# Kernel tuning notes

Measured on AMD Instinct MI355X. Metric: run time of the kernel, lower is better.

The kernel has to match this reference:

```python
import jax, jax.numpy as jnp
import numpy as np

B, L, S = 128, 80, 8          # dialogues, utterances per dialogue, speakers
NODE_DIM, HIDDEN, HEADS, OUT_DIM = 768, 512, 8, 256
N = B * L


def _build_edges():
    """Replicates InterSentenceGNN.build_graph + Batch.from_data_list offsets."""
    rel = np.zeros((N, 3), np.float32)
    all_e, last = [], []
    eye3 = np.eye(3, dtype=np.float32)
    for b in range(B):
        off = b * L
        u = L - 1
        e, t = [], []
        for i in range(L):
            if i > 0:
                e += [[i - 1, i], [i, i - 1]]; t += [0, 0]   # REL_SEQ
            if i < u:
                e += [[i, u], [u, i]]; t += [1, 1]           # REL_CTX
        for s in range(S):                                   # REL_SPK, round-robin speakers
            g = list(range(s, L, S))
            for a in range(len(g)):
                for c in range(a + 1, len(g)):
                    e += [[g[a], g[c]], [g[c], g[a]]]; t += [2, 2]
        e = np.asarray(e, np.int64); t = np.asarray(t, np.int64)
        np.add.at(rel, e[:, 0] + off, eye3[t])               # out-degree per relation (pre-unique)
        all_e.append(np.unique(e, axis=0) + off)             # torch.unique(idx, dim=1)
        last.append(off + u)
    edge_index = np.concatenate(all_e, 0).T.astype(np.int32)  # [2, E], row0=src, row1=dst
    return edge_index, rel, np.asarray(last, np.int32)


def setup_inputs() -> dict:
    key = jax.random.key(0)
    ks = jax.random.split(key, 16)
    edge_index, rel_feat, last_idx = _build_edges()
    g = lambda k, shp, fan: jax.random.normal(k, shp, jnp.float32) * (1.0 / np.sqrt(fan))
    return {
        "x": jax.random.normal(ks[0], (N, NODE_DIM), jnp.float32),
        "rel_feat": jnp.asarray(rel_feat),
        "w1": g(ks[1], (3, 64), 3), "b1": jnp.zeros((64,), jnp.float32),
        "w2": g(ks[2], (64, 1), 64), "b2": jnp.zeros((1,), jnp.float32),
        "Wl1": g(ks[3], (NODE_DIM, HIDDEN), NODE_DIM), "bl1": jnp.zeros((HIDDEN,), jnp.float32),
        "Wr1": g(ks[4], (NODE_DIM, HIDDEN), NODE_DIM), "br1": jnp.zeros((HIDDEN,), jnp.float32),
        "att1": g(ks[5], (HEADS, HIDDEN // HEADS), HIDDEN // HEADS),
        "bias1": jnp.zeros((HIDDEN,), jnp.float32),
        "Wl2": g(ks[6], (HIDDEN, OUT_DIM), HIDDEN), "bl2": jnp.zeros((OUT_DIM,), jnp.float32),
        "Wr2": g(ks[7], (HIDDEN, OUT_DIM), HIDDEN), "br2": jnp.zeros((OUT_DIM,), jnp.float32),
        "att2": g(ks[8], (1, OUT_DIM), OUT_DIM),
        "bias2": jnp.zeros((OUT_DIM,), jnp.float32),
        "ln_g": jnp.ones((OUT_DIM,), jnp.float32), "ln_b": jnp.zeros((OUT_DIM,), jnp.float32),
        "edge_index": jnp.asarray(edge_index),
        "last_idx": jnp.asarray(last_idx),
    }


def _gatv2(x, Wl, bl, Wr, br, att, bias, src, dst, heads, ch, concat):
    """PyG GATv2Conv (eval mode, self-loops already in src/dst)."""
    n = x.shape[0]
    xl = (x @ Wl + bl).reshape(n, heads, ch)   # source transform (messages)
    xr = (x @ Wr + br).reshape(n, heads, ch)   # target transform
    e = jax.nn.leaky_relu(xl[src] + xr[dst], negative_slope=0.2)  # [E,H,C]
    logit = jnp.einsum("ehc,hc->eh", e, att)                      # [E,H]
    m = jax.ops.segment_max(logit, dst, num_segments=n)
    a = jnp.exp(logit - m[dst])
    denom = jax.ops.segment_sum(a, dst, num_segments=n)
    alpha = a / denom[dst]                                        # segment softmax over dst
    msg = (xl[src] * alpha[:, :, None]).reshape(-1, heads * ch)
    out = jax.ops.segment_sum(msg, dst, num_segments=n).reshape(n, heads, ch)
    out = out.reshape(n, heads * ch) if concat else out.mean(axis=1)
    return out + bias


def reference(x, rel_feat, w1, b1, w2, b2, Wl1, bl1, Wr1, br1, att1, bias1,
              Wl2, bl2, Wr2, br2, att2, bias2, ln_g, ln_b, edge_index, last_idx):
    n = x.shape[0]
    loops = jnp.arange(n, dtype=edge_index.dtype)
    src = jnp.concatenate([edge_index[0], loops])  # add_self_loops=True (PyG default)
    dst = jnp.concatenate([edge_index[1], loops])
    w = jax.nn.sigmoid(jax.nn.relu(rel_feat @ w1 + b1) @ w2 + b2)  # [N,1] node gate
    h = x * w
    h = jax.nn.elu(_gatv2(h, Wl1, bl1, Wr1, br1, att1, bias1, src, dst, HEADS, HIDDEN // HEADS, True))
    h = _gatv2(h, Wl2, bl2, Wr2, br2, att2, bias2, src, dst, 1, OUT_DIM, False)
    mu = jnp.mean(h, axis=-1, keepdims=True)
    var = jnp.mean((h - mu) ** 2, axis=-1, keepdims=True)
    h = (h - mu) * jax.lax.rsqrt(var + 1e-5) * ln_g + ln_b
    return h[last_idx]  # x[batch.ptr[1:] - 1]: last (context) node per dialogue
```

## Files before the change

### kernel.cpp

```cpp
#include <hip/hip_runtime.h>
#include <hip/hip_bf16.h>

#define NN 10240
#define LL 80
#define BB 128

typedef _Float16 half8 __attribute__((ext_vector_type(8)));
typedef _Float16 half2v __attribute__((ext_vector_type(2)));
typedef float f32x4 __attribute__((ext_vector_type(4)));

#define GLD16(gptr, lptr)                                                        \
  __builtin_amdgcn_global_load_lds(                                              \
      (const __attribute__((address_space(1))) void*)(gptr),                     \
      (__attribute__((address_space(3))) void*)(lptr), 16, 0, 0)

__device__ __forceinline__ float dot2f(half2v a, half2v b, float c) {
#if __has_builtin(__builtin_amdgcn_fdot2)
  return __builtin_amdgcn_fdot2(a, b, c, false);
#else
  return c + (float)a.x * (float)b.x + (float)a.y * (float)b.y;
#endif
}
__device__ __forceinline__ half2v u2h(unsigned int u) { half2v r; __builtin_memcpy(&r, &u, 4); return r; }
__device__ __forceinline__ unsigned int h2u(half2v h) { unsigned int u; __builtin_memcpy(&u, &h, 4); return u; }
__device__ __forceinline__ unsigned int dupf16(float v) {
  _Float16 hv = (_Float16)v;
  unsigned short u; __builtin_memcpy(&u, &hv, 2);
  return (unsigned int)u * 0x10001u;
}

__global__ __launch_bounds__(256) void prep_all(
    const float* __restrict__ x, const float* __restrict__ rel,
    const float* __restrict__ w1, const float* __restrict__ b1,
    const float* __restrict__ w2, const float* __restrict__ b2,
    const float* __restrict__ Wl1, const float* __restrict__ Wr1,
    const float* __restrict__ Wl2, const float* __restrict__ Wr2,
    const float* __restrict__ bl1, const float* __restrict__ br1,
    const float* __restrict__ att1,
    _Float16* __restrict__ h0, _Float16* __restrict__ Wt1,
    _Float16* __restrict__ Wt2cat,
    float* __restrict__ biasc, _Float16* __restrict__ att_h) {
  __shared__ float tile[32][33];
  int bid = blockIdx.x;
  int tid = threadIdx.x;
  if (bid < NN) {
    int n = bid;
    __shared__ float s_w;
    if (tid < 64) {
      float r0 = rel[n * 3 + 0], r1 = rel[n * 3 + 1], r2 = rel[n * 3 + 2];
      float v = r0 * w1[tid] + r1 * w1[64 + tid] + r2 * w1[128 + tid] + b1[tid];
      v = v > 0.f ? v : 0.f;
      v *= w2[tid];
      for (int d = 32; d; d >>= 1) v += __shfl_down(v, d, 64);
      if (tid == 0) s_w = 1.f / (1.f + __expf(-(v + b2[0])));
    }
    __syncthreads();
    float w = s_w;
    const float* xr = x + (size_t)n * 768;
    _Float16* hr = h0 + (size_t)n * 768;
    for (int c = tid; c < 768; c += 256) hr[c] = (_Float16)(xr[c] * w);
    return;
  }
  int r = bid - NN;
  const float* W;
  _Float16* Wt;
  int K, Nc, bx, by;
  if (r < 384)      { W = Wl1; Wt = Wt1;                          K = 768; Nc = 512; bx = r % 16;       by = r / 16; }
  else if (r < 768) { W = Wr1; Wt = Wt1 + (size_t)512 * 768;      K = 768; Nc = 512; bx = (r-384) % 16; by = (r-384) / 16; }
  else if (r < 896) { W = Wl2; Wt = Wt2cat;                       K = 512; Nc = 256; bx = (r-768) % 8;  by = (r-768) / 8; }
  else if (r < 1024){ W = Wr2; Wt = Wt2cat + (size_t)256 * 512;   K = 512; Nc = 256; bx = (r-896) % 8;  by = (r-896) / 8; }
  else {
    for (int i = tid; i < 1024; i += 256) biasc[i] = (i < 512) ? bl1[i] : br1[i - 512];
    for (int i = tid; i < 512; i += 256) att_h[i] = (_Float16)att1[i];
    return;
  }
  int n0 = bx * 32, k0 = by * 32;
  int c = tid & 31, rr = tid >> 5;
#pragma unroll
  for (int p = 0; p < 4; ++p) {
    int rw = p * 8 + rr;
    tile[rw][c] = W[(size_t)(k0 + rw) * Nc + n0 + c];
  }
  __syncthreads();
#pragma unroll
  for (int p = 0; p < 4; ++p) {
    int rw = p * 8 + rr;
    Wt[(size_t)(n0 + rw) * K + k0 + c] = (_Float16)tile[c][rw];
  }
}

__global__ __launch_bounds__(256) void gemm_mfma(
    const _Float16* __restrict__ A, const _Float16* __restrict__ Bt,
    const float* __restrict__ bias, _Float16* __restrict__ Cout,
    int K, int Nc) {
  __shared__ __align__(16) _Float16 As[128 * 32];
  __shared__ __align__(16) _Float16 Bs[128 * 32];
  int bm = blockIdx.y * 128, bn = blockIdx.x * 128;
  int tid = threadIdx.x;
  int wave = tid >> 6, lane = tid & 63;
  int wm = (wave & 1) * 64, wn = (wave >> 1) * 64;
  int lr = lane & 15, lk = lane >> 4;
  int r0 = tid >> 2, sg = tid & 3;
  const _Float16* aP0 = A + (size_t)(bm + r0) * K + sg * 8;
  const _Float16* aP1 = A + (size_t)(bm + 64 + r0) * K + sg * 8;
  const _Float16* bP0 = Bt + (size_t)(bn + r0) * K + sg * 8;
  const _Float16* bP1 = Bt + (size_t)(bn + 64 + r0) * K + sg * 8;
  int lds0 = (tid & ~63) * 8;
  f32x4 acc[4][4] = {};
  for (int k0 = 0; k0 < K; k0 += 32) {
    GLD16(aP0 + k0, As + lds0);
    GLD16(aP1 + k0, As + lds0 + 2048);
    GLD16(bP0 + k0, Bs + lds0);
    GLD16(bP1 + k0, Bs + lds0 + 2048);
    __syncthreads();
    half8 af[4], bfv[4];
#pragma unroll
    for (int i = 0; i < 4; ++i)
      af[i] = *(const half8*)(As + (wm + i * 16 + lr) * 32 + lk * 8);
#pragma unroll
    for (int j = 0; j < 4; ++j)
      bfv[j] = *(const half8*)(Bs + (wn + j * 16 + lr) * 32 + lk * 8);
#pragma unroll
    for (int i = 0; i < 4; ++i)
#pragma unroll
      for (int j = 0; j < 4; ++j)
        acc[i][j] = __builtin_amdgcn_mfma_f32_16x16x32_f16(af[i], bfv[j], acc[i][j], 0, 0, 0);
    __syncthreads();
  }
#pragma unroll
  for (int i = 0; i < 4; ++i)
#pragma unroll
    for (int j = 0; j < 4; ++j)
#pragma unroll
      for (int rg = 0; rg < 4; ++rg) {
        int row = bm + wm + i * 16 + lk * 4 + rg;
        int col = bn + wn + j * 16 + lr;
        Cout[(size_t)row * Nc + col] = (_Float16)(acc[i][j][rg] + bias[col]);
      }
}

#define PB 66
__global__ __launch_bounds__(512) void gat1_fused(
    const _Float16* __restrict__ xlr, const _Float16* __restrict__ att_h,
    const float* __restrict__ bias1, _Float16* __restrict__ h1) {
  __shared__ _Float16 s_xl[80 * PB];
  __shared__ _Float16 s_xr[80 * PB];
  __shared__ float s_logit[16 * 81];
  __shared__ unsigned int s_al[16 * 81];
  __shared__ short s_src[16 * 81];
  __shared__ short s_cnt[80];
  __shared__ float s_hub[80];
  __shared__ unsigned int s_hub16[80];
  __shared__ unsigned int s_hp[16][32];
  int bx = blockIdx.x;
  int h = bx & 7, b = bx >> 3;
  int base = b * LL;
  int tid = threadIdx.x;

  for (int idx = tid; idx < 1280; idx += 512) {
    bool isxr = idx >= 640;
    int lidx = isxr ? idx - 640 : idx;
    int row = lidx >> 3, ch = lidx & 7;
    const _Float16* gp = xlr + (size_t)(base + row) * 1024 + (isxr ? 512 : 0) + h * 64 + ch * 8;
    uint4 g = *(const uint4*)gp;
    _Float16* sp = (isxr ? s_xr : s_xl) + row * PB + ch * 8;
    ((unsigned int*)sp)[0] = g.x;
    ((unsigned int*)sp)[1] = g.y;
    ((unsigned int*)sp)[2] = g.z;
    ((unsigned int*)sp)[3] = g.w;
  }
  if (tid < 79) {
    int d = tid;
    int list[16];
    int c = 0;
    list[c++] = d;
    if (d > 0) list[c++] = d - 1;
    if (d + 1 < 79) list[c++] = d + 1;
    list[c++] = 79;
    for (int j = d & 7; j < 80; j += 8)
      if (j != d && j != 79) list[c++] = j;
    s_cnt[d] = (short)c;
    for (int i = c; i < 16; ++i) list[i] = -1;
#pragma unroll
    for (int i = 0; i < 16; ++i) s_src[i * 81 + d] = (short)list[i];
  }
  __syncthreads();

  const unsigned int* pat = (const unsigned int*)(att_h + h * 64);
  const half2v c02 = {(_Float16)0.2f, (_Float16)0.2f};
  for (int s = tid; s < 1344; s += 512) {
    int d, src;
    bool ishub = s >= 1264;
    if (!ishub) { d = s >> 4; src = s_src[(s & 15) * 81 + d]; }
    else { d = 79; src = s - 1264; }
    int ssrc = src < 0 ? 0 : src;
    const unsigned int* pa = (const unsigned int*)(s_xl + ssrc * PB);
    const unsigned int* pb = (const unsigned int*)(s_xr + d * PB);
    float acc = 0.f;
#pragma unroll
    for (int q = 0; q < 16; ++q) {
      unsigned int a0 = pa[2 * q], a1 = pa[2 * q + 1];
      unsigned int b0 = pb[2 * q], b1 = pb[2 * q + 1];
      half2v at0 = u2h(__builtin_amdgcn_readfirstlane(pat[2 * q]));
      half2v at1 = u2h(__builtin_amdgcn_readfirstlane(pat[2 * q + 1]));
      half2v e0 = u2h(a0) + u2h(b0);
      half2v e1 = u2h(a1) + u2h(b1);
      half2v l0 = __builtin_elementwise_max(e0, e0 * c02);
      half2v l1 = __builtin_elementwise_max(e1, e1 * c02);
      acc = dot2f(l0, at0, acc);
      acc = dot2f(l1, at1, acc);
    }
    if (!ishub) s_logit[(s & 15) * 81 + d] = (src < 0) ? -3e38f : acc;
    else s_hub[src] = acc;
  }
  __syncthreads();

  if (tid < 79) {
    int d = tid;
    float m = -3e38f, v[16];
#pragma unroll
    for (int i = 0; i < 16; ++i) { v[i] = s_logit[i * 81 + d]; m = fmaxf(m, v[i]); }
    float sum = 0.f;
#pragma unroll
    for (int i = 0; i < 16; ++i) { v[i] = __expf(v[i] - m); sum += v[i]; }
    float inv = 1.f / sum;
#pragma unroll
    for (int i = 0; i < 16; ++i) s_al[i * 81 + d] = dupf16(v[i] * inv);
  } else if (tid >= 448) {
    int l = tid - 448;
    float v0 = s_hub[l];
    float v1 = (l < 16) ? s_hub[64 + l] : -3e38f;
    float m = fmaxf(v0, v1);
    for (int d = 32; d; d >>= 1) m = fmaxf(m, __shfl_xor(m, d, 64));
    float e0 = __expf(v0 - m);
    float e1 = (l < 16) ? __expf(v1 - m) : 0.f;
    float sum = e0 + e1;
    for (int d = 32; d; d >>= 1) sum += __shfl_xor(sum, d, 64);
    float inv = 1.f / sum;
    s_hub16[l] = dupf16(e0 * inv);
    if (l < 16) s_hub16[64 + l] = dupf16(e1 * inv);
  }
  __syncthreads();

  int qw = tid >> 4, l = tid & 15;
  int c0 = l * 4;
#pragma unroll
  for (int k = 0; k < 3; ++k) {
    int d = qw + 32 * k;
    if (d >= 79) continue;
    int cnt = s_cnt[d];
    half2v a0 = {(_Float16)0.f, (_Float16)0.f};
    half2v a1 = a0;
    for (int i = 0; i < cnt; ++i) {
      int src = s_src[i * 81 + d];
      half2v al = u2h(s_al[i * 81 + d]);
      const unsigned int* px = (const unsigned int*)(s_xl + src * PB + c0);
      a0 += al * u2h(px[0]);
      a1 += al * u2h(px[1]);
    }
    float v0 = (float)a0.x + bias1[h * 64 + c0];
    float v1 = (float)a0.y + bias1[h * 64 + c0 + 1];
    float v2 = (float)a1.x + bias1[h * 64 + c0 + 2];
    float v3 = (float)a1.y + bias1[h * 64 + c0 + 3];
    v0 = v0 > 0.f ? v0 : __expf(v0) - 1.f;
    v1 = v1 > 0.f ? v1 : __expf(v1) - 1.f;
    v2 = v2 > 0.f ? v2 : __expf(v2) - 1.f;
    v3 = v3 > 0.f ? v3 : __expf(v3) - 1.f;
    half2v o0 = {(_Float16)v0, (_Float16)v1};
    half2v o1 = {(_Float16)v2, (_Float16)v3};
    uint2 ov = {h2u(o0), h2u(o1)};
    *(uint2*)&h1[(size_t)(base + d) * 512 + h * 64 + c0] = ov;
  }
  if (qw >= 16) {
    int g = qw - 16;
    half2v a0 = {(_Float16)0.f, (_Float16)0.f};
    half2v a1 = a0;
#pragma unroll
    for (int s5 = 0; s5 < 5; ++s5) {
      int src = g * 5 + s5;
      half2v al = u2h(s_hub16[src]);
      const unsigned int* px = (const unsigned int*)(s_xl + src * PB + c0);
      a0 += al * u2h(px[0]);
      a1 += al * u2h(px[1]);
    }
    s_hp[g][2 * l] = h2u(a0);
    s_hp[g][2 * l + 1] = h2u(a1);
  }
  __syncthreads();
  if (tid < 32) {
    float f0 = 0.f, f1 = 0.f;
#pragma unroll
    for (int g = 0; g < 16; ++g) {
      half2v v = u2h(s_hp[g][tid]);
      f0 += (float)v.x;
      f1 += (float)v.y;
    }
    int c = tid * 2;
    float v0 = f0 + bias1[h * 64 + c];
    float v1 = f1 + bias1[h * 64 + c + 1];
    v0 = v0 > 0.f ? v0 : __expf(v0) - 1.f;
    v1 = v1 > 0.f ? v1 : __expf(v1) - 1.f;
    half2v o = {(_Float16)v0, (_Float16)v1};
    *(unsigned int*)&h1[(size_t)(base + 79) * 512 + h * 64 + c] = h2u(o);
  }
}

#define PX 266
__global__ __launch_bounds__(512) void gemm2gat2(
    const _Float16* __restrict__ h1, const _Float16* __restrict__ Bt,
    const float* __restrict__ bl2, const float* __restrict__ br2,
    const float* __restrict__ att2, const float* __restrict__ bias2,
    const float* __restrict__ ln_g, const float* __restrict__ ln_b,
    float* __restrict__ out) {
  __shared__ __align__(16) char smem[80 * PX * 2];
  __shared__ _Float16 s_att[256];
  __shared__ _Float16 s_xr[256];
  __shared__ float s_red[80];
  __shared__ float s_sum[4], s_sq[4];
  _Float16* As = (_Float16*)smem;
  _Float16* Bs = (_Float16*)(smem + 5120);
  _Float16* s_x = (_Float16*)smem;

  int b = blockIdx.x;
  int tid = threadIdx.x;
  int wave = tid >> 6, lane = tid & 63;
  int lr = lane & 15, lk = lane >> 4;

  if (tid < 256) s_att[tid] = (_Float16)att2[tid];

  int achunk = wave * 64 + lane;
  const _Float16* aP = h1 + (size_t)(b * 80 + (achunk >> 2)) * 512 + (achunk & 3) * 8;
  const _Float16* bP[4];
#pragma unroll
  for (int j = 0; j < 4; ++j) {
    int c = wave * 256 + j * 64 + lane;
    bP[j] = Bt + (size_t)(c >> 2) * 512 + (c & 3) * 8;
  }
  f32x4 acc[5][4] = {};
  for (int k0 = 0; k0 < 512; k0 += 32) {
    if (wave < 5) GLD16(aP + k0, As + (size_t)achunk * 8 - (size_t)lane * 8 + lane * 8);
#pragma unroll
    for (int j = 0; j < 4; ++j)
      GLD16(bP[j] + k0, Bs + (wave * 256 + j * 64) * 8 + lane * 8);
    __syncthreads();
    half8 af[5], bfv;
#pragma unroll
    for (int i = 0; i < 5; ++i)
      af[i] = *(const half8*)(As + (i * 16 + lr) * 32 + lk * 8);
#pragma unroll
    for (int j = 0; j < 4; ++j) {
      bfv = *(const half8*)(Bs + (wave * 64 + j * 16 + lr) * 32 + lk * 8);
#pragma unroll
      for (int i = 0; i < 5; ++i)
        acc[i][j] = __builtin_amdgcn_mfma_f32_16x16x32_f16(af[i], bfv, acc[i][j], 0, 0, 0);
    }
    __syncthreads();
  }
  if (wave < 4) {
#pragma unroll
    for (int i = 0; i < 5; ++i)
#pragma unroll
      for (int j = 0; j < 4; ++j)
#pragma unroll
        for (int rg = 0; rg < 4; ++rg) {
          int row = i * 16 + lk * 4 + rg;
          int col = wave * 64 + j * 16 + lr;
          s_x[row * PX + col] = (_Float16)(acc[i][j][rg] + bl2[col]);
        }
  } else if (lk == 3) {
#pragma unroll
    for (int j = 0; j < 4; ++j) {
      int colx = (wave - 4) * 64 + j * 16 + lr;
      s_xr[colx] = (_Float16)(acc[4][j][3] + br2[colx]);
    }
  }
  __syncthreads();
  if (tid < 160) {
    int r = tid >> 1, hf = tid & 1;
    const half2v* xa = (const half2v*)(s_x + r * PX + hf * 128);
    const half2v* xr = (const half2v*)(s_xr + hf * 128);
    const half2v* at = (const half2v*)(s_att + hf * 128);
    float lg = 0.f;
    const half2v c02 = {(_Float16)0.2f, (_Float16)0.2f};
#pragma unroll
    for (int q = 0; q < 64; ++q) {
      half2v e = xa[q] + xr[q];
      half2v l = __builtin_elementwise_max(e, e * c02);
      lg = dot2f(l, at[q], lg);
    }
    lg += __shfl_xor(lg, 1, 64);
    if (hf == 0) s_red[r] = lg;
  }
  __syncthreads();
  if (wave == 7) {
    float v0 = s_red[lane];
    float v1 = (lane < 16) ? s_red[64 + lane] : -3e38f;
    float m = fmaxf(v0, v1);
    for (int d = 32; d; d >>= 1) m = fmaxf(m, __shfl_xor(m, d, 64));
    float e0 = __expf(v0 - m);
    float e1 = (lane < 16) ? __expf(v1 - m) : 0.f;
    float sum = e0 + e1;
    for (int d = 32; d; d >>= 1) sum += __shfl_xor(sum, d, 64);
    float inv = 1.f / sum;
    s_red[lane] = e0 * inv;
    if (lane < 16) s_red[64 + lane] = e1 * inv;
  }
  __syncthreads();
  float v = 0.f;
  if (tid < 256) {
    float a = 0.f;
#pragma unroll
    for (int r = 0; r < 80; ++r) a += s_red[r] * (float)s_x[r * PX + tid];
    v = a + bias2[tid];
    float p = v;
    for (int d = 32; d; d >>= 1) p += __shfl_down(p, d, 64);
    if (lane == 0) s_sum[wave] = p;
    float q = v * v;
    for (int d = 32; d; d >>= 1) q += __shfl_down(q, d, 64);
    if (lane == 0) s_sq[wave] = q;
  }
  __syncthreads();
  if (tid < 256) {
    float mu = (s_sum[0] + s_sum[1] + s_sum[2] + s_sum[3]) * (1.f / 256.f);
    float ex2 = (s_sq[0] + s_sq[1] + s_sq[2] + s_sq[3]) * (1.f / 256.f);
    float var = ex2 - mu * mu;
    float r = rsqrtf(var + 1e-5f);
    out[b * 256 + tid] = (v - mu) * r * ln_g[tid] + ln_b[tid];
  }
}

extern "C" void kernel_launch(void* const* d_in, const int* in_sizes, int n_in,
                              void* d_out, int out_size, void* d_ws, size_t ws_size,
                              hipStream_t stream) {
  const float* x      = (const float*)d_in[0];
  const float* rel    = (const float*)d_in[1];
  const float* w1     = (const float*)d_in[2];
  const float* b1     = (const float*)d_in[3];
  const float* w2     = (const float*)d_in[4];
  const float* b2     = (const float*)d_in[5];
  const float* Wl1    = (const float*)d_in[6];
  const float* bl1    = (const float*)d_in[7];
  const float* Wr1    = (const float*)d_in[8];
  const float* br1    = (const float*)d_in[9];
  const float* att1   = (const float*)d_in[10];
  const float* bias1  = (const float*)d_in[11];
  const float* Wl2    = (const float*)d_in[12];
  const float* bl2    = (const float*)d_in[13];
  const float* Wr2    = (const float*)d_in[14];
  const float* br2    = (const float*)d_in[15];
  const float* att2   = (const float*)d_in[16];
  const float* bias2  = (const float*)d_in[17];
  const float* ln_g   = (const float*)d_in[18];
  const float* ln_b   = (const float*)d_in[19];
  float* out = (float*)d_out;

  char* p = (char*)d_ws;
  _Float16* h0     = (_Float16*)p; p += (size_t)NN * 768 * 2;
  _Float16* h1     = (_Float16*)p; p += (size_t)NN * 512 * 2;
  _Float16* Wt1    = (_Float16*)p; p += (size_t)1024 * 768 * 2;
  _Float16* Wt2cat = (_Float16*)p; p += (size_t)512 * 512 * 2;
  _Float16* att_h  = (_Float16*)p; p += 1024;
  float* biasc     = (float*)p; p += 1024 * 4;
  _Float16* xlr    = (_Float16*)p; p += (size_t)NN * 1024 * 2;

  prep_all<<<NN + 1025, 256, 0, stream>>>(x, rel, w1, b1, w2, b2, Wl1, Wr1, Wl2, Wr2,
                                          bl1, br1, att1, h0, Wt1, Wt2cat, biasc, att_h);

  gemm_mfma<<<dim3(8, 80), 256, 0, stream>>>(h0, Wt1, biasc, xlr, 768, 1024);

  gat1_fused<<<1024, 512, 0, stream>>>(xlr, att_h, bias1, h1);

  gemm2gat2<<<BB, 512, 0, stream>>>(h1, Wt2cat, bl2, br2, att2, bias2, ln_g, ln_b, out);
}
```

Before: 197.8 us.

## Compute GAT1 aggregation as dense attention-matrix MFMA instead of sparse gather

Replaces the per-destination sparse gather-accumulate in gat1_fused with a dense 80x96 attention probability matrix P in shared memory, multiplied by a transposed copy of xl using 16x16x32 f16 MFMA. Softmax results are scattered into P, and the hub node (node 79) is handled as an ordinary row, which removes the separate partial-sum reduction pass. The intent is to cut scalar half2 FMA work and irregular LDS reads. In exchange it adds a transposed xl staging copy, zero-fills P, and does dense multiplies over mostly-zero entries, with only 4 of 8 waves doing the MFMA.

New measurement: 200.1 us. No clear change (+1.1%).

```diff
diff --git a/kernel.cpp b/kernel.cpp
--- a/kernel.cpp
+++ b/kernel.cpp
@@ -22,12 +22,6 @@
 #endif
 }
 __device__ __forceinline__ half2v u2h(unsigned int u) { half2v r; __builtin_memcpy(&r, &u, 4); return r; }
-__device__ __forceinline__ unsigned int h2u(half2v h) { unsigned int u; __builtin_memcpy(&u, &h, 4); return u; }
-__device__ __forceinline__ unsigned int dupf16(float v) {
-  _Float16 hv = (_Float16)v;
-  unsigned short u; __builtin_memcpy(&u, &hv, 2);
-  return (unsigned int)u * 0x10001u;
-}
 
 __global__ __launch_bounds__(256) void prep_all(
     const float* __restrict__ x, const float* __restrict__ rel,
@@ -140,18 +134,19 @@
 }
 
 #define PB 66
+#define PT 104
 __global__ __launch_bounds__(512) void gat1_fused(
     const _Float16* __restrict__ xlr, const _Float16* __restrict__ att_h,
     const float* __restrict__ bias1, _Float16* __restrict__ h1) {
-  __shared__ _Float16 s_xl[80 * PB];
-  __shared__ _Float16 s_xr[80 * PB];
-  __shared__ float s_logit[16 * 81];
-  __shared__ unsigned int s_al[16 * 81];
-  __shared__ short s_src[16 * 81];
-  __shared__ short s_cnt[80];
-  __shared__ float s_hub[80];
-  __shared__ unsigned int s_hub16[80];
-  __shared__ unsigned int s_hp[16][32];
+  __shared__ __align__(16) char smem[48768];
+  _Float16* s_xl  = (_Float16*)smem;
+  _Float16* s_xlT = (_Float16*)(smem + 10560);
+  _Float16* s_xr  = (_Float16*)(smem + 23872);
+  _Float16* s_P   = (_Float16*)(smem + 23872);
+  float* s_logit  = (float*)(smem + 40512);
+  short* s_src    = (short*)(smem + 45696);
+  short* s_cnt    = (short*)(smem + 48288);
+  float* s_hub    = (float*)(smem + 48448);
   int bx = blockIdx.x;
   int h = bx & 7, b = bx >> 3;
   int base = b * LL;
@@ -168,6 +163,20 @@
     ((unsigned int*)sp)[1] = g.y;
     ((unsigned int*)sp)[2] = g.z;
     ((unsigned int*)sp)[3] = g.w;
+    if (!isxr) {
+      _Float16 vals[8];
+      __builtin_memcpy(vals, &g, 16);
+      int c0 = ch * 8;
+#pragma unroll
+      for (int jj = 0; jj < 8; ++jj) {
+        int j = (jj + tid) & 7;
+        s_xlT[(c0 + j) * PT + row] = vals[j];
+      }
+    }
+  }
+  {
+    int r = tid >> 3, o = tid & 7;
+    *(unsigned int*)(s_xlT + r * PT + 80 + o * 2) = 0u;
   }
   if (tid < 79) {
     int d = tid;
@@ -215,18 +224,21 @@
   }
   __syncthreads();
 
+  float v[16];
+  float inv = 0.f;
+  int cnt = 0;
   if (tid < 79) {
-    int d = tid;
-    float m = -3e38f, v[16];
-#pragma unroll
-    for (int i = 0; i < 16; ++i) { v[i] = s_logit[i * 81 + d]; m = fmaxf(m, v[i]); }
+    cnt = s_cnt[tid];
+    float m = -3e38f;
+#pragma unroll
+    for (int i = 0; i < 16; ++i) { v[i] = s_logit[i * 81 + tid]; m = fmaxf(m, v[i]); }
     float sum = 0.f;
 #pragma unroll
     for (int i = 0; i < 16; ++i) { v[i] = __expf(v[i] - m); sum += v[i]; }
-    float inv = 1.f / sum;
-#pragma unroll
-    for (int i = 0; i < 16; ++i) s_al[i * 81 + d] = dupf16(v[i] * inv);
-  } else if (tid >= 448) {
+    inv = 1.f / sum;
+  }
+  float he0 = 0.f, he1 = 0.f;
+  if (tid >= 448) {
     int l = tid - 448;
     float v0 = s_hub[l];
     float v1 = (l < 16) ? s_hub[64 + l] : -3e38f;
@@ -236,72 +248,51 @@
     float e1 = (l < 16) ? __expf(v1 - m) : 0.f;
     float sum = e0 + e1;
     for (int d = 32; d; d >>= 1) sum += __shfl_xor(sum, d, 64);
-    float inv = 1.f / sum;
-    s_hub16[l] = dupf16(e0 * inv);
-    if (l < 16) s_hub16[64 + l] = dupf16(e1 * inv);
-  }
-  __syncthreads();
-
-  int qw = tid >> 4, l = tid & 15;
-  int c0 = l * 4;
-#pragma unroll
-  for (int k = 0; k < 3; ++k) {
-    int d = qw + 32 * k;
-    if (d >= 79) continue;
-    int cnt = s_cnt[d];
-    half2v a0 = {(_Float16)0.f, (_Float16)0.f};
-    half2v a1 = a0;
-    for (int i = 0; i < cnt; ++i) {
-      int src = s_src[i * 81 + d];
-      half2v al = u2h(s_al[i * 81 + d]);
-      const unsigned int* px = (const unsigned int*)(s_xl + src * PB + c0);
-      a0 += al * u2h(px[0]);
-      a1 += al * u2h(px[1]);
-    }
-    float v0 = (float)a0.x + bias1[h * 64 + c0];
-    float v1 = (float)a0.y + bias1[h * 64 + c0 + 1];
-    float v2 = (float)a1.x + bias1[h * 64 + c0 + 2];
-    float v3 = (float)a1.y + bias1[h * 64 + c0 + 3];
-    v0 = v0 > 0.f ? v0 : __expf(v0) - 1.f;
-    v1 = v1 > 0.f ? v1 : __expf(v1) - 1.f;
-    v2 = v2 > 0.f ? v2 : __expf(v2) - 1.f;
-    v3 = v3 > 0.f ? v3 : __expf(v3) - 1.f;
-    half2v o0 = {(_Float16)v0, (_Float16)v1};
-    half2v o1 = {(_Float16)v2, (_Float16)v3};
-    uint2 ov = {h2u(o0), h2u(o1)};
-    *(uint2*)&h1[(size_t)(base + d) * 512 + h * 64 + c0] = ov;
-  }
-  if (qw >= 16) {
-    int g = qw - 16;
-    half2v a0 = {(_Float16)0.f, (_Float16)0.f};
-    half2v a1 = a0;
-#pragma unroll
-    for (int s5 = 0; s5 < 5; ++s5) {
-      int src = g * 5 + s5;
-      half2v al = u2h(s_hub16[src]);
-      const unsigned int* px = (const unsigned int*)(s_xl + src * PB + c0);
-      a0 += al * u2h(px[0]);
-      a1 += al * u2h(px[1]);
-    }
-    s_hp[g][2 * l] = h2u(a0);
-    s_hp[g][2 * l + 1] = h2u(a1);
-  }
-  __syncthreads();
-  if (tid < 32) {
-    float f0 = 0.f, f1 = 0.f;
-#pragma unroll
-    for (int g = 0; g < 16; ++g) {
-      half2v v = u2h(s_hp[g][tid]);
-      f0 += (float)v.x;
-      f1 += (float)v.y;
-    }
-    int c = tid * 2;
-    float v0 = f0 + bias1[h * 64 + c];
-    float v1 = f1 + bias1[h * 64 + c + 1];
-    v0 = v0 > 0.f ? v0 : __expf(v0) - 1.f;
-    v1 = v1 > 0.f ? v1 : __expf(v1) - 1.f;
-    half2v o = {(_Float16)v0, (_Float16)v1};
-    *(unsigned int*)&h1[(size_t)(base + 79) * 512 + h * 64 + c] = h2u(o);
+    float sinv = 1.f / sum;
+    he0 = e0 * sinv;
+    he1 = e1 * sinv;
+  }
+  for (int i = tid; i < 2080; i += 512) {
+    uint2 z; z.x = 0u; z.y = 0u;
+    ((uint2*)s_P)[i] = z;
+  }
+  __syncthreads();
+
+  if (tid < 79) {
+    for (int i = 0; i < cnt; ++i)
+      s_P[tid * PT + s_src[i * 81 + tid]] = (_Float16)(v[i] * inv);
+  }
+  if (tid >= 448) {
+    int l = tid - 448;
+    s_P[79 * PT + l] = (_Float16)he0;
+    if (l < 16) s_P[79 * PT + 64 + l] = (_Float16)he1;
+  }
+  __syncthreads();
+
+  int wv = tid >> 6, lane = tid & 63;
+  int lr = lane & 15, lk = lane >> 4;
+  if (wv < 4) {
+    f32x4 acc[5] = {};
+#pragma unroll
+    for (int k = 0; k < 3; ++k) {
+      half8 bf = *(const half8*)(s_xlT + (wv * 16 + lr) * PT + k * 32 + lk * 8);
+#pragma unroll
+      for (int m = 0; m < 5; ++m) {
+        half8 af = *(const half8*)(s_P + (m * 16 + lr) * PT + k * 32 + lk * 8);
+        acc[m] = __builtin_amdgcn_mfma_f32_16x16x32_f16(af, bf, acc[m], 0, 0, 0);
+      }
+    }
+    int c = wv * 16 + lr;
+    float bb = bias1[h * 64 + c];
+#pragma unroll
+    for (int m = 0; m < 5; ++m)
+#pragma unroll
+      for (int rg = 0; rg < 4; ++rg) {
+        int dd = m * 16 + lk * 4 + rg;
+        float val = acc[m][rg] + bb;
+        val = val > 0.f ? val : __expf(val) - 1.f;
+        h1[(size_t)(base + dd) * 512 + h * 64 + c] = (_Float16)val;
+      }
   }
 }
 
```

## Fuse first-layer projection GEMM into per-dialogue-head GAT1 kernel

Applied to the files above, without the earlier changes.

Removes the standalone tiled GEMM that wrote the full xl/xr projection to global memory. Each (dialogue, head) block now computes its own 80x128 slice of the projection with MFMA straight into shared memory, then runs attention on it. This drops the intermediate global write and read round trip and one kernel launch. In exchange each block has a tiny GEMM with one B tile per wave and low MFMA reuse, so the A rows are reloaded once per head, eight times in total. Shared memory is aliased between the GEMM tiles and the logit buffers to keep occupancy.

New measurement: 194.7 us. About the same (-1.6%).

```diff
diff --git a/kernel.cpp b/kernel.cpp
--- a/kernel.cpp
+++ b/kernel.cpp
@@ -89,85 +89,67 @@
   }
 }
 
-__global__ __launch_bounds__(256) void gemm_mfma(
-    const _Float16* __restrict__ A, const _Float16* __restrict__ Bt,
-    const float* __restrict__ bias, _Float16* __restrict__ Cout,
-    int K, int Nc) {
-  __shared__ __align__(16) _Float16 As[128 * 32];
-  __shared__ __align__(16) _Float16 Bs[128 * 32];
-  int bm = blockIdx.y * 128, bn = blockIdx.x * 128;
-  int tid = threadIdx.x;
-  int wave = tid >> 6, lane = tid & 63;
-  int wm = (wave & 1) * 64, wn = (wave >> 1) * 64;
-  int lr = lane & 15, lk = lane >> 4;
-  int r0 = tid >> 2, sg = tid & 3;
-  const _Float16* aP0 = A + (size_t)(bm + r0) * K + sg * 8;
-  const _Float16* aP1 = A + (size_t)(bm + 64 + r0) * K + sg * 8;
-  const _Float16* bP0 = Bt + (size_t)(bn + r0) * K + sg * 8;
-  const _Float16* bP1 = Bt + (size_t)(bn + 64 + r0) * K + sg * 8;
-  int lds0 = (tid & ~63) * 8;
-  f32x4 acc[4][4] = {};
-  for (int k0 = 0; k0 < K; k0 += 32) {
-    GLD16(aP0 + k0, As + lds0);
-    GLD16(aP1 + k0, As + lds0 + 2048);
-    GLD16(bP0 + k0, Bs + lds0);
-    GLD16(bP1 + k0, Bs + lds0 + 2048);
-    __syncthreads();
-    half8 af[4], bfv[4];
-#pragma unroll
-    for (int i = 0; i < 4; ++i)
-      af[i] = *(const half8*)(As + (wm + i * 16 + lr) * 32 + lk * 8);
-#pragma unroll
-    for (int j = 0; j < 4; ++j)
-      bfv[j] = *(const half8*)(Bs + (wn + j * 16 + lr) * 32 + lk * 8);
-#pragma unroll
-    for (int i = 0; i < 4; ++i)
-#pragma unroll
-      for (int j = 0; j < 4; ++j)
-        acc[i][j] = __builtin_amdgcn_mfma_f32_16x16x32_f16(af[i], bfv[j], acc[i][j], 0, 0, 0);
-    __syncthreads();
-  }
-#pragma unroll
-  for (int i = 0; i < 4; ++i)
-#pragma unroll
-    for (int j = 0; j < 4; ++j)
-#pragma unroll
-      for (int rg = 0; rg < 4; ++rg) {
-        int row = bm + wm + i * 16 + lk * 4 + rg;
-        int col = bn + wn + j * 16 + lr;
-        Cout[(size_t)row * Nc + col] = (_Float16)(acc[i][j][rg] + bias[col]);
-      }
-}
-
 #define PB 66
-__global__ __launch_bounds__(512) void gat1_fused(
-    const _Float16* __restrict__ xlr, const _Float16* __restrict__ att_h,
+__global__ __launch_bounds__(512, 8) void gemm1gat1(
+    const _Float16* __restrict__ h0, const _Float16* __restrict__ Wt1,
+    const float* __restrict__ biasc, const _Float16* __restrict__ att_h,
     const float* __restrict__ bias1, _Float16* __restrict__ h1) {
-  __shared__ _Float16 s_xl[80 * PB];
-  __shared__ _Float16 s_xr[80 * PB];
-  __shared__ float s_logit[16 * 81];
-  __shared__ unsigned int s_al[16 * 81];
-  __shared__ short s_src[16 * 81];
-  __shared__ short s_cnt[80];
-  __shared__ float s_hub[80];
-  __shared__ unsigned int s_hub16[80];
-  __shared__ unsigned int s_hp[16][32];
+  __shared__ __align__(16) char smem[36928];
+  _Float16* s_xl = (_Float16*)smem;
+  _Float16* s_xr = (_Float16*)(smem + 10560);
+  _Float16* As   = (_Float16*)(smem + 21120);
+  _Float16* Bs   = (_Float16*)(smem + 26240);
+  float* s_logit = (float*)(smem + 21120);
+  unsigned int* s_al = (unsigned int*)(smem + 26304);
+  short* s_src   = (short*)(smem + 31488);
+  short* s_cnt   = (short*)(smem + 34080);
+  float* s_hub   = (float*)(smem + 34240);
+  unsigned int* s_hub16 = (unsigned int*)(smem + 34560);
+  unsigned int* s_hp = (unsigned int*)(smem + 34880);
+
   int bx = blockIdx.x;
   int h = bx & 7, b = bx >> 3;
   int base = b * LL;
   int tid = threadIdx.x;
-
-  for (int idx = tid; idx < 1280; idx += 512) {
-    bool isxr = idx >= 640;
-    int lidx = isxr ? idx - 640 : idx;
-    int row = lidx >> 3, ch = lidx & 7;
-    const _Float16* gp = xlr + (size_t)(base + row) * 1024 + (isxr ? 512 : 0) + h * 64 + ch * 8;
-    uint4 g = *(const uint4*)gp;
-    _Float16* sp = (isxr ? s_xr : s_xl) + row * PB + ch * 8;
-    ((unsigned int*)sp)[0] = g.x;
-    ((unsigned int*)sp)[1] = g.y;
-    ((unsigned int*)sp)[2] = g.z;
-    ((unsigned int*)sp)[3] = g.w;
+  int wave = tid >> 6, lane = tid & 63;
+  int lr = lane & 15, lk = lane >> 4;
+
+  const _Float16* aP = h0;
+  if (wave < 5) {
+    int c = wave * 64 + lane;
+    aP = h0 + (size_t)(base + (c >> 2)) * 768 + (c & 3) * 8;
+  }
+  int cB = wave * 64 + lane;
+  int brow = cB >> 2;
+  int wrow = (brow < 64) ? (h * 64 + brow) : (512 + h * 64 + (brow - 64));
+  const _Float16* bP = Wt1 + (size_t)wrow * 768 + (cB & 3) * 8;
+
+  f32x4 acc[5] = {};
+  for (int k0 = 0; k0 < 768; k0 += 32) {
+    if (wave < 5) GLD16(aP + k0, As + wave * 512);
+    GLD16(bP + k0, Bs + wave * 512);
+    __syncthreads();
+    half8 bf = *(const half8*)(Bs + (wave * 16 + lr) * 32 + lk * 8);
+#pragma unroll
+    for (int m = 0; m < 5; ++m) {
+      half8 af = *(const half8*)(As + (m * 16 + lr) * 32 + lk * 8);
+      acc[m] = __builtin_amdgcn_mfma_f32_16x16x32_f16(af, bf, acc[m], 0, 0, 0);
+    }
+    __syncthreads();
+  }
+  {
+    int c = wave * 16 + lr;
+    bool isxl = c < 64;
+    int cc = isxl ? c : c - 64;
+    float bb = biasc[(isxl ? 0 : 512) + h * 64 + cc];
+    _Float16* dst = isxl ? s_xl : s_xr;
+#pragma unroll
+    for (int m = 0; m < 5; ++m)
+#pragma unroll
+      for (int rg = 0; rg < 4; ++rg) {
+        int row = m * 16 + lk * 4 + rg;
+        dst[row * PB + cc] = (_Float16)(acc[m][rg] + bb);
+      }
   }
   if (tid < 79) {
     int d = tid;
@@ -196,7 +178,7 @@
     int ssrc = src < 0 ? 0 : src;
     const unsigned int* pa = (const unsigned int*)(s_xl + ssrc * PB);
     const unsigned int* pb = (const unsigned int*)(s_xr + d * PB);
-    float acc = 0.f;
+    float acc2 = 0.f;
 #pragma unroll
     for (int q = 0; q < 16; ++q) {
       unsigned int a0 = pa[2 * q], a1 = pa[2 * q + 1];
@@ -207,11 +189,11 @@
       half2v e1 = u2h(a1) + u2h(b1);
       half2v l0 = __builtin_elementwise_max(e0, e0 * c02);
       half2v l1 = __builtin_elementwise_max(e1, e1 * c02);
-      acc = dot2f(l0, at0, acc);
-      acc = dot2f(l1, at1, acc);
-    }
-    if (!ishub) s_logit[(s & 15) * 81 + d] = (src < 0) ? -3e38f : acc;
-    else s_hub[src] = acc;
+      acc2 = dot2f(l0, at0, acc2);
+      acc2 = dot2f(l1, at1, acc2);
+    }
+    if (!ishub) s_logit[(s & 15) * 81 + d] = (src < 0) ? -3e38f : acc2;
+    else s_hub[src] = acc2;
   }
   __syncthreads();
 
@@ -283,15 +265,15 @@
       a0 += al * u2h(px[0]);
       a1 += al * u2h(px[1]);
     }
-    s_hp[g][2 * l] = h2u(a0);
-    s_hp[g][2 * l + 1] = h2u(a1);
+    s_hp[g * 32 + 2 * l] = h2u(a0);
+    s_hp[g * 32 + 2 * l + 1] = h2u(a1);
   }
   __syncthreads();
   if (tid < 32) {
     float f0 = 0.f, f1 = 0.f;
 #pragma unroll
     for (int g = 0; g < 16; ++g) {
-      half2v v = u2h(s_hp[g][tid]);
+      half2v v = u2h(s_hp[g * 32 + tid]);
       f0 += (float)v.x;
       f1 += (float)v.y;
     }
@@ -338,10 +320,10 @@
   }
   f32x4 acc[5][4] = {};
   for (int k0 = 0; k0 < 512; k0 += 32) {
-    if (wave < 5) GLD16(aP + k0, As + (size_t)achunk * 8 - (size_t)lane * 8 + lane * 8);
+    if (wave < 5) GLD16(aP + k0, As + wave * 512);
 #pragma unroll
     for (int j = 0; j < 4; ++j)
-      GLD16(bP[j] + k0, Bs + (wave * 256 + j * 64) * 8 + lane * 8);
+      GLD16(bP[j] + k0, Bs + (wave * 256 + j * 64) * 8);
     __syncthreads();
     half8 af[5], bfv;
 #pragma unroll
@@ -461,14 +443,11 @@
   _Float16* Wt2cat = (_Float16*)p; p += (size_t)512 * 512 * 2;
   _Float16* att_h  = (_Float16*)p; p += 1024;
   float* biasc     = (float*)p; p += 1024 * 4;
-  _Float16* xlr    = (_Float16*)p; p += (size_t)NN * 1024 * 2;
 
   prep_all<<<NN + 1025, 256, 0, stream>>>(x, rel, w1, b1, w2, b2, Wl1, Wr1, Wl2, Wr2,
                                           bl1, br1, att1, h0, Wt1, Wt2cat, biasc, att_h);
 
-  gemm_mfma<<<dim3(8, 80), 256, 0, stream>>>(h0, Wt1, biasc, xlr, 768, 1024);
-
-  gat1_fused<<<1024, 512, 0, stream>>>(xlr, att_h, bias1, h1);
+  gemm1gat1<<<1024, 512, 0, stream>>>(h0, Wt1, biasc, att_h, bias1, h1);
 
   gemm2gat2<<<BB, 512, 0, stream>>>(h1, Wt2cat, bl2, br2, att2, bias2, ln_g, ln_b, out);
 }
```
